# Performance work log

Hardware: AMD Instinct MI355X
Metric: run time of the kernel (lower is better)

## Reference

```python
import jax, jax.numpy as jnp
import numpy as np

ALPHA = 0.2  # LeakyReLU negative slope


def setup_inputs() -> dict:
    key = jax.random.key(0)
    k1, k2, k3, k4 = jax.random.split(key, 4)
    B, N, Fin, Fout = 8, 2048, 256, 256
    h = jax.random.normal(k1, (B, N, Fin), dtype=jnp.float32)
    # random 0/1 adjacency with guaranteed self-loops so every row has a neighbor
    adj = jax.random.randint(k2, (N, N), 0, 2).astype(jnp.float32)
    adj = jnp.maximum(adj, jnp.eye(N, dtype=jnp.float32))
    # xavier_uniform with gain=1.414
    def xavier(k, shape, gain=1.414):
        fan_in, fan_out = shape[0], shape[1]
        a = gain * np.sqrt(6.0 / (fan_in + fan_out))
        return jax.random.uniform(k, shape, dtype=jnp.float32, minval=-a, maxval=a)
    W = xavier(k3, (Fin, Fout))
    a = xavier(k4, (2 * Fout, 1))
    return {"h": h, "adj_matrix": adj, "W": W, "a": a}


def reference(h, adj_matrix, W, a):
    # h: [B, N, Fin], adj_matrix: [N, N], W: [Fin, Fout], a: [2*Fout, 1]
    Fout = W.shape[1]
    Wh = jnp.einsum("bnf,fo->bno", h, W)            # [B, N, Fout]
    a1, a2 = a[:Fout, 0], a[Fout:, 0]                 # split additive attention vector
    # e[b,i,j] = leakyrelu(Wh[b,i]@a1 + Wh[b,j]@a2) — equals concat([Wh_i,Wh_j])@a
    s1 = Wh @ a1                                      # [B, N]
    s2 = Wh @ a2                                      # [B, N]
    e = s1[:, :, None] + s2[:, None, :]               # [B, N, N]
    e = jnp.where(e >= 0, e, ALPHA * e)               # LeakyReLU
    e = jnp.where(adj_matrix[None] == 0, -jnp.inf, e)  # mask non-edges
    attention = jax.nn.softmax(e, axis=-1)            # [B, N, N]
    # dropout is identity in eval mode (training=False)
    h_prime = jnp.einsum("bij,bjo->bio", attention, Wh)
    return h_prime
```

## Files before the change

### kernel.cpp

```cpp
#include <hip/hip_runtime.h>
#include <cstdint>

#define NN 2048
#define LOG2E 1.4426950408889634f

typedef __attribute__((ext_vector_type(8))) short bf16x8;
typedef __attribute__((ext_vector_type(4))) float f32x4;

__device__ __forceinline__ unsigned short f2bf(float x){
  union { float f; unsigned u; } v; v.f = x;
  unsigned r = v.u + 0x7FFFu + ((v.u >> 16) & 1u);
  return (unsigned short)(r >> 16);
}
__device__ __forceinline__ unsigned pack2(float a, float b){
  return (unsigned)f2bf(a) | ((unsigned)f2bf(b) << 16);
}
__device__ __forceinline__ unsigned permpack(unsigned hi, unsigned lo){
  return __builtin_amdgcn_perm(hi, lo, 0x07060302u);
}

__global__ __launch_bounds__(256) void k_prep(const float* __restrict__ adj,
                                              const float* __restrict__ W,
                                              unsigned long long* __restrict__ ab,
                                              unsigned short* __restrict__ Wt){
  const int tid = threadIdx.x;
  const int bid = blockIdx.x;
  if (bid < 512){
    const int lane = tid & 63;
    unsigned* ab32 = (unsigned*)ab;
    #pragma unroll
    for (int r = 0; r < 4; r++){
      const int row = bid * 4 + r;
      #pragma unroll
      for (int part = 0; part < 2; part++){
        float4 v = ((const float4*)(adj + (size_t)row * NN))[part * 256 + tid];
        unsigned n = (v.x != 0.f ? 1u : 0u) | (v.y != 0.f ? 2u : 0u)
                   | (v.z != 0.f ? 4u : 0u) | (v.w != 0.f ? 8u : 0u);
        unsigned m;
        m = __shfl_xor(n, 1); n = (lane & 1) ? (m | (n << 4))  : (n | (m << 4));
        m = __shfl_xor(n, 2); n = (lane & 2) ? (m | (n << 8))  : (n | (m << 8));
        m = __shfl_xor(n, 4); n = (lane & 4) ? (m | (n << 16)) : (n | (m << 16));
        if ((lane & 7) == 0)
          ab32[row * 64 + part * 32 + (tid >> 3)] = n;
      }
    }
  } else {
    int g = (bid - 512) * 256 + tid;
    int o = g >> 8, k = g & 255;
    Wt[g] = f2bf(W[k * 256 + o]);
  }
}

__global__ __launch_bounds__(512, 2) void k_fused_gemm(const float* __restrict__ h,
                                                       const unsigned short* __restrict__ Wt,
                                                       const float* __restrict__ a,
                                                       unsigned short* __restrict__ WhT,
                                                       float* __restrict__ s1c,
                                                       float* __restrict__ s2c){
  __shared__ __align__(16) unsigned char As[2 * 8192];
  __shared__ __align__(16) unsigned short Ts[256 * 72];
  __shared__ float s1p[8][64], s2p[8][64];
  const int tid = threadIdx.x;
  const int r0 = blockIdx.x * 64;
  const int b  = r0 >> 11;
  const int i0 = r0 & (NN - 1);
  const int w = tid >> 6, lane = tid & 63, lhi = lane >> 4, llo = lane & 15;
  const int wc = w * 32;
  const int sit = w >> 1, skk = w & 1;
  const int srow = sit * 16 + llo;
  const int skol = skk * 32 + lhi * 8;

  f32x4 acc[4][2];
  #pragma unroll
  for (int i = 0; i < 4; i++)
    #pragma unroll
    for (int j = 0; j < 2; j++){ acc[i][j][0]=0.f; acc[i][j][1]=0.f; acc[i][j][2]=0.f; acc[i][j][3]=0.f; }

  float4 hv[4][2];
  #pragma unroll
  for (int t = 0; t < 4; t++){
    const float* hp = h + (size_t)(r0 + srow) * 256 + t * 64 + skol;
    hv[t][0] = *(const float4*)hp;
    hv[t][1] = *(const float4*)(hp + 4);
  }

  auto loadB = [&](int k0, bf16x8* dst){
    #pragma unroll
    for (int ot = 0; ot < 2; ot++)
      #pragma unroll
      for (int kk = 0; kk < 2; kk++)
        dst[ot * 2 + kk] = *(const bf16x8*)(Wt + (size_t)(wc + ot * 16 + llo) * 256 + k0 + kk * 32 + lhi * 8);
  };
  bf16x8 bfr[2][4];
  loadB(0, bfr[0]);

  #pragma unroll
  for (int t = 0; t < 4; t++){
    uint4 q = make_uint4(pack2(hv[t][0].x, hv[t][0].y), pack2(hv[t][0].z, hv[t][0].w),
                         pack2(hv[t][1].x, hv[t][1].y), pack2(hv[t][1].z, hv[t][1].w));
    *(uint4*)&As[(t & 1) * 8192 + w * 1024 + lane * 16] = q;
    __syncthreads();
    if (t < 3) loadB((t + 1) * 64, bfr[(t + 1) & 1]);
    bf16x8 af[2][4];
    #pragma unroll
    for (int kk = 0; kk < 2; kk++)
      #pragma unroll
      for (int it = 0; it < 4; it++)
        af[kk][it] = *(const bf16x8*)&As[(t & 1) * 8192 + (it * 2 + kk) * 1024 + lane * 16];
    #pragma unroll
    for (int kk = 0; kk < 2; kk++)
      #pragma unroll
      for (int it = 0; it < 4; it++)
        #pragma unroll
        for (int ot = 0; ot < 2; ot++)
          acc[it][ot] = __builtin_amdgcn_mfma_f32_16x16x32_bf16(af[kk][it], bfr[t & 1][ot * 2 + kk], acc[it][ot], 0, 0, 0);
  }

  float a1v[2], a2v[2];
  #pragma unroll
  for (int ot = 0; ot < 2; ot++){
    a1v[ot] = a[wc + ot * 16 + llo] * LOG2E;
    a2v[ot] = a[256 + wc + ot * 16 + llo] * LOG2E;
  }
  #pragma unroll
  for (int it = 0; it < 4; it++){
    #pragma unroll
    for (int q = 0; q < 4; q++){
      float p1 = acc[it][0][q] * a1v[0] + acc[it][1][q] * a1v[1];
      float p2 = acc[it][0][q] * a2v[0] + acc[it][1][q] * a2v[1];
      #pragma unroll
      for (int o = 1; o < 16; o <<= 1){ p1 += __shfl_xor(p1, o); p2 += __shfl_xor(p2, o); }
      if (llo == 0){
        s1p[w][it * 16 + lhi * 4 + q] = p1;
        s2p[w][it * 16 + lhi * 4 + q] = p2;
      }
    }
  }

  #pragma unroll
  for (int it = 0; it < 4; it++){
    #pragma unroll
    for (int ot = 0; ot < 2; ot++){
      int o = wc + ot * 16 + llo;
      uint2 u = make_uint2(pack2(acc[it][ot][0], acc[it][ot][1]),
                           pack2(acc[it][ot][2], acc[it][ot][3]));
      *(uint2*)&Ts[o * 72 + it * 16 + lhi * 4] = u;
    }
  }
  __syncthreads();

  if (tid < 64){
    float t1 = 0.f, t2 = 0.f;
    #pragma unroll
    for (int g = 0; g < 8; g++){ t1 += s1p[g][tid]; t2 += s2p[g][tid]; }
    s1c[r0 + tid] = t1;
    s2c[r0 + tid] = t2;
  }
  #pragma unroll
  for (int p = 0; p < 4; p++){
    int o = p * 64 + (tid >> 3), col = (tid & 7) * 8;
    *(uint4*)(WhT + (size_t)(b * 256 + o) * 2048 + i0 + col) = *(const uint4*)&Ts[o * 72 + col];
  }
}

__global__ __launch_bounds__(512, 2) void k_attn(const float* __restrict__ s1c,
                                                 const float* __restrict__ s2c,
                                                 const unsigned short* __restrict__ WhT,
                                                 const unsigned long long* __restrict__ ab,
                                                 float* __restrict__ out){
  __shared__ __align__(16) float E1s[2048];
  __shared__ __align__(16) float E2s[2048];
  __shared__ __align__(16) unsigned char PsB[2 * 16384];
  __shared__ __align__(16) unsigned char bitsB[64 * 264];
  __shared__ float s1s[64], lin[64], red[8], rsp[8][64];
  const int tid = threadIdx.x;
  const int bid = blockIdx.x;
  const int b = bid & 7, i0 = (bid >> 3) * 64;
  const int w = tid >> 6, lane = tid & 63, lhi = lane >> 4, llo = lane & 15;
  const int wc = w * 32;
  const int sit = w >> 1, skk = w & 1;
  const int sfrag = sit * 2 + skk;
  const int prow = sit * 16 + llo;

  float4 v = ((const float4*)(s2c + (size_t)b * NN))[tid];
  ((float4*)E1s)[tid] = make_float4(__builtin_amdgcn_exp2f(v.x), __builtin_amdgcn_exp2f(v.y),
                                    __builtin_amdgcn_exp2f(v.z), __builtin_amdgcn_exp2f(v.w));
  ((float4*)E2s)[tid] = make_float4(__builtin_amdgcn_exp2f(0.2f * v.x), __builtin_amdgcn_exp2f(0.2f * v.y),
                                    __builtin_amdgcn_exp2f(0.2f * v.z), __builtin_amdgcn_exp2f(0.2f * v.w));
  float vmax = fmaxf(fmaxf(v.x, v.y), fmaxf(v.z, v.w));
  #pragma unroll
  for (int o = 32; o; o >>= 1) vmax = fmaxf(vmax, __shfl_xor(vmax, o));
  if (lane == 0) red[w] = vmax;
  if (tid < 64) s1s[tid] = s1c[(size_t)b * NN + i0 + tid];
  #pragma unroll
  for (int k = 0; k < 4; k++){
    int g = k * 512 + tid;
    unsigned long long mw = ab[(size_t)i0 * 32 + g];
    *(unsigned long long*)&bitsB[(g >> 5) * 264 + (g & 31) * 8] = mw;
  }
  __syncthreads();
  float m2 = red[0];
  #pragma unroll
  for (int g = 1; g < 8; g++) m2 = fmaxf(m2, red[g]);

  const float s1v = s1s[prow];
  const float xm = s1v + m2;
  const float mv = fmaxf(xm, 0.2f * xm);
  const float k1 = __builtin_amdgcn_exp2f(s1v - mv);
  const float k2 = __builtin_amdgcn_exp2f(0.2f * s1v - mv);
  float rs = 0.f;

  f32x4 acc[4][2];
  #pragma unroll
  for (int i = 0; i < 4; i++)
    #pragma unroll
    for (int j = 0; j < 2; j++){ acc[i][j][0]=0.f; acc[i][j][1]=0.f; acc[i][j][2]=0.f; acc[i][j][3]=0.f; }

  auto loadB = [&](int j0, bf16x8* dst){
    #pragma unroll
    for (int jh = 0; jh < 2; jh++)
      #pragma unroll
      for (int ot = 0; ot < 2; ot++)
        #pragma unroll
        for (int kk = 0; kk < 2; kk++)
          dst[jh * 4 + ot * 2 + kk] = *(const bf16x8*)(WhT + (size_t)(b * 256 + wc + ot * 16 + llo) * 2048 + j0 + jh * 64 + kk * 32 + lhi * 8);
  };

  unsigned puq[8];
  auto computeP = [&](int tn, unsigned* pq){
    unsigned bits = bitsB[prow * 264 + tn * 8 + skk * 4 + lhi];
    const int off = tn * 64 + skk * 32 + lhi * 8;
    float4 xa = *(const float4*)&E1s[off];
    float4 xb = *(const float4*)&E1s[off + 4];
    float4 ya = *(const float4*)&E2s[off];
    float4 yb = *(const float4*)&E2s[off + 4];
    float e1[8] = {xa.x, xa.y, xa.z, xa.w, xb.x, xb.y, xb.z, xb.w};
    float e2[8] = {ya.x, ya.y, ya.z, ya.w, yb.x, yb.y, yb.z, yb.w};
    unsigned pu[8];
    #pragma unroll
    for (int e = 0; e < 8; e++){
      float p = fmaxf(e1[e] * k1, e2[e] * k2);
      unsigned m = ((bits >> e) & 1u) ? 0xFFFF0000u : 0u;
      unsigned u = __float_as_uint(p) & m;
      rs += __uint_as_float(u);
      pu[e] = u;
    }
    pq[0] = permpack(pu[1], pu[0]); pq[1] = permpack(pu[3], pu[2]);
    pq[2] = permpack(pu[5], pu[4]); pq[3] = permpack(pu[7], pu[6]);
  };

  auto stageBody = [&](int t, int BUF, bf16x8* curB, bf16x8* nxtB, bool last){
    *(uint4*)&PsB[BUF * 16384 +        sfrag * 1024 + lane * 16] = *(uint4*)&puq[0];
    *(uint4*)&PsB[BUF * 16384 + 8192 + sfrag * 1024 + lane * 16] = *(uint4*)&puq[4];
    __syncthreads();
    if (!last) loadB((t + 1) * 128, nxtB);
    bf16x8 af[2][4];
    #pragma unroll
    for (int kk = 0; kk < 2; kk++)
      #pragma unroll
      for (int it = 0; it < 4; it++)
        af[kk][it] = *(const bf16x8*)&PsB[BUF * 16384 + (it * 2 + kk) * 1024 + lane * 16];
    if (!last) computeP(2 * (t + 1), &puq[0]);
    #pragma unroll
    for (int kk = 0; kk < 2; kk++)
      #pragma unroll
      for (int it = 0; it < 4; it++)
        #pragma unroll
        for (int ot = 0; ot < 2; ot++)
          acc[it][ot] = __builtin_amdgcn_mfma_f32_16x16x32_bf16(af[kk][it], curB[ot * 2 + kk], acc[it][ot], 0, 0, 0);
    #pragma unroll
    for (int kk = 0; kk < 2; kk++)
      #pragma unroll
      for (int it = 0; it < 4; it++)
        af[kk][it] = *(const bf16x8*)&PsB[BUF * 16384 + 8192 + (it * 2 + kk) * 1024 + lane * 16];
    if (!last) computeP(2 * (t + 1) + 1, &puq[4]);
    #pragma unroll
    for (int kk = 0; kk < 2; kk++)
      #pragma unroll
      for (int it = 0; it < 4; it++)
        #pragma unroll
        for (int ot = 0; ot < 2; ot++)
          acc[it][ot] = __builtin_amdgcn_mfma_f32_16x16x32_bf16(af[kk][it], curB[4 + ot * 2 + kk], acc[it][ot], 0, 0, 0);
  };

  bf16x8 bA[8], bB[8];
  loadB(0, bA);
  computeP(0, &puq[0]);
  computeP(1, &puq[4]);
  for (int t2 = 0; t2 < 16; t2 += 2){
    stageBody(t2,     0, bA, bB, false);
    stageBody(t2 + 1, 1, bB, bA, t2 + 1 == 15);
  }

  rs += __shfl_xor(rs, 16);
  rs += __shfl_xor(rs, 32);
  if (lhi == 0) rsp[w][prow] = rs;
  __syncthreads();
  if (tid < 64){
    int it = tid >> 4;
    lin[tid] = 1.0f / (rsp[it * 2][tid] + rsp[it * 2 + 1][tid]);
  }
  __syncthreads();

  #pragma unroll
  for (int it = 0; it < 4; it++){
    #pragma unroll
    for (int ot = 0; ot < 2; ot++){
      int col = wc + ot * 16 + llo;
      #pragma unroll
      for (int q = 0; q < 4; q++){
        int row = it * 16 + lhi * 4 + q;
        out[(size_t)(b * NN + i0 + row) * 256 + col] = acc[it][ot][q] * lin[row];
      }
    }
  }
}

extern "C" void kernel_launch(void* const* d_in, const int* in_sizes, int n_in,
                              void* d_out, int out_size, void* d_ws, size_t ws_size,
                              hipStream_t stream) {
  const float* h   = (const float*)d_in[0];
  const float* adj = (const float*)d_in[1];
  const float* W   = (const float*)d_in[2];
  const float* a   = (const float*)d_in[3];
  float* out = (float*)d_out;

  char* ws = (char*)d_ws;
  unsigned short* WhT      = (unsigned short*)(ws);
  unsigned short* Wt       = (unsigned short*)(ws + 8388608);
  unsigned long long* ab   = (unsigned long long*)(ws + 8519680);
  float* s1c               = (float*)(ws + 9043968);
  float* s2c               = (float*)(ws + 9109504);

  hipLaunchKernelGGL(k_prep,       dim3(768), dim3(256), 0, stream, adj, W, ab, Wt);
  hipLaunchKernelGGL(k_fused_gemm, dim3(256), dim3(512), 0, stream, h, Wt, a, WhT, s1c, s2c);
  hipLaunchKernelGGL(k_attn,       dim3(256), dim3(512), 0, stream, s1c, s2c, WhT, ab, out);
}
```

Baseline: 132.7 us.

## Stage 512 attention columns per barrier and prioritize MFMA issue

The P-tile staging buffer in shared memory grows to hold 512 key columns at once, so the block synchronizes 4 times instead of 16. Eight P fragments are computed per stage and kept in registers, while WhT fragments are double-buffered at 64-column granularity. The first B load is hoisted above the prologue, and s_setprio raises wave priority around the MFMA bursts. In exchange it uses much more LDS (64KB for Ps) and more registers for puq, which could limit occupancy or cause spills.

After: 130.9 us. No clear change (-1.4%).

```diff
diff --git a/kernel.cpp b/kernel.cpp
--- a/kernel.cpp
+++ b/kernel.cpp
@@ -170,7 +170,7 @@
                                                  float* __restrict__ out){
   __shared__ __align__(16) float E1s[2048];
   __shared__ __align__(16) float E2s[2048];
-  __shared__ __align__(16) unsigned char PsB[2 * 16384];
+  __shared__ __align__(16) unsigned char Ps[65536];
   __shared__ __align__(16) unsigned char bitsB[64 * 264];
   __shared__ float s1s[64], lin[64], red[8], rsp[8][64];
   const int tid = threadIdx.x;
@@ -182,6 +182,16 @@
   const int sfrag = sit * 2 + skk;
   const int prow = sit * 16 + llo;
 
+  auto loadB = [&](int j0, bf16x8* dst){
+    #pragma unroll
+    for (int ot = 0; ot < 2; ot++)
+      #pragma unroll
+      for (int kk = 0; kk < 2; kk++)
+        dst[ot * 2 + kk] = *(const bf16x8*)(WhT + (size_t)(b * 256 + wc + ot * 16 + llo) * 2048 + j0 + kk * 32 + lhi * 8);
+  };
+  bf16x8 bA[4], bB[4];
+  loadB(0, bA);
+
   float4 v = ((const float4*)(s2c + (size_t)b * NN))[tid];
   ((float4*)E1s)[tid] = make_float4(__builtin_amdgcn_exp2f(v.x), __builtin_amdgcn_exp2f(v.y),
                                     __builtin_amdgcn_exp2f(v.z), __builtin_amdgcn_exp2f(v.w));
@@ -216,24 +226,14 @@
     #pragma unroll
     for (int j = 0; j < 2; j++){ acc[i][j][0]=0.f; acc[i][j][1]=0.f; acc[i][j][2]=0.f; acc[i][j][3]=0.f; }
 
-  auto loadB = [&](int j0, bf16x8* dst){
-    #pragma unroll
-    for (int jh = 0; jh < 2; jh++)
-      #pragma unroll
-      for (int ot = 0; ot < 2; ot++)
-        #pragma unroll
-        for (int kk = 0; kk < 2; kk++)
-          dst[jh * 4 + ot * 2 + kk] = *(const bf16x8*)(WhT + (size_t)(b * 256 + wc + ot * 16 + llo) * 2048 + j0 + jh * 64 + kk * 32 + lhi * 8);
-  };
-
-  unsigned puq[8];
-  auto computeP = [&](int tn, unsigned* pq){
-    unsigned bits = bitsB[prow * 264 + tn * 8 + skk * 4 + lhi];
-    const int off = tn * 64 + skk * 32 + lhi * 8;
-    float4 xa = *(const float4*)&E1s[off];
-    float4 xb = *(const float4*)&E1s[off + 4];
-    float4 ya = *(const float4*)&E2s[off];
-    float4 yb = *(const float4*)&E2s[off + 4];
+  unsigned puq[32];
+  auto computeP = [&](int sN, int jc, unsigned* pq){
+    const int j0 = sN * 512 + jc * 64 + skk * 32 + lhi * 8;
+    unsigned bits = bitsB[prow * 264 + (j0 >> 3)];
+    float4 xa = *(const float4*)&E1s[j0];
+    float4 xb = *(const float4*)&E1s[j0 + 4];
+    float4 ya = *(const float4*)&E2s[j0];
+    float4 yb = *(const float4*)&E2s[j0 + 4];
     float e1[8] = {xa.x, xa.y, xa.z, xa.w, xb.x, xb.y, xb.z, xb.w};
     float e2[8] = {ya.x, ya.y, ya.z, ya.w, yb.x, yb.y, yb.z, yb.w};
     unsigned pu[8];
@@ -249,47 +249,38 @@
     pq[2] = permpack(pu[5], pu[4]); pq[3] = permpack(pu[7], pu[6]);
   };
 
-  auto stageBody = [&](int t, int BUF, bf16x8* curB, bf16x8* nxtB, bool last){
-    *(uint4*)&PsB[BUF * 16384 +        sfrag * 1024 + lane * 16] = *(uint4*)&puq[0];
-    *(uint4*)&PsB[BUF * 16384 + 8192 + sfrag * 1024 + lane * 16] = *(uint4*)&puq[4];
+  #pragma unroll
+  for (int jc = 0; jc < 8; jc++) computeP(0, jc, &puq[jc * 4]);
+
+  for (int s = 0; s < 4; s++){
+    if (s) __syncthreads();
+    #pragma unroll
+    for (int jc = 0; jc < 8; jc++)
+      *(uint4*)&Ps[jc * 8192 + sfrag * 1024 + lane * 16] = *(const uint4*)&puq[jc * 4];
     __syncthreads();
-    if (!last) loadB((t + 1) * 128, nxtB);
-    bf16x8 af[2][4];
-    #pragma unroll
-    for (int kk = 0; kk < 2; kk++)
-      #pragma unroll
-      for (int it = 0; it < 4; it++)
-        af[kk][it] = *(const bf16x8*)&PsB[BUF * 16384 + (it * 2 + kk) * 1024 + lane * 16];
-    if (!last) computeP(2 * (t + 1), &puq[0]);
-    #pragma unroll
-    for (int kk = 0; kk < 2; kk++)
-      #pragma unroll
-      for (int it = 0; it < 4; it++)
+    #pragma unroll
+    for (int jc = 0; jc < 8; jc++){
+      bf16x8 af[2][4];
+      #pragma unroll
+      for (int kk = 0; kk < 2; kk++)
         #pragma unroll
-        for (int ot = 0; ot < 2; ot++)
-          acc[it][ot] = __builtin_amdgcn_mfma_f32_16x16x32_bf16(af[kk][it], curB[ot * 2 + kk], acc[it][ot], 0, 0, 0);
-    #pragma unroll
-    for (int kk = 0; kk < 2; kk++)
-      #pragma unroll
-      for (int it = 0; it < 4; it++)
-        af[kk][it] = *(const bf16x8*)&PsB[BUF * 16384 + 8192 + (it * 2 + kk) * 1024 + lane * 16];
-    if (!last) computeP(2 * (t + 1) + 1, &puq[4]);
-    #pragma unroll
-    for (int kk = 0; kk < 2; kk++)
-      #pragma unroll
-      for (int it = 0; it < 4; it++)
+        for (int it = 0; it < 4; it++)
+          af[kk][it] = *(const bf16x8*)&Ps[jc * 8192 + (it * 2 + kk) * 1024 + lane * 16];
+      bf16x8* cur = (jc & 1) ? bB : bA;
+      bf16x8* nxt = (jc & 1) ? bA : bB;
+      if (jc < 7)       loadB((s * 8 + jc + 1) * 64, nxt);
+      else if (s < 3)   loadB((s + 1) * 512, nxt);
+      if (s < 3) computeP(s + 1, jc, &puq[jc * 4]);
+      __builtin_amdgcn_s_setprio(1);
+      #pragma unroll
+      for (int kk = 0; kk < 2; kk++)
         #pragma unroll
-        for (int ot = 0; ot < 2; ot++)
-          acc[it][ot] = __builtin_amdgcn_mfma_f32_16x16x32_bf16(af[kk][it], curB[4 + ot * 2 + kk], acc[it][ot], 0, 0, 0);
-  };
-
-  bf16x8 bA[8], bB[8];
-  loadB(0, bA);
-  computeP(0, &puq[0]);
-  computeP(1, &puq[4]);
-  for (int t2 = 0; t2 < 16; t2 += 2){
-    stageBody(t2,     0, bA, bB, false);
-    stageBody(t2 + 1, 1, bB, bA, t2 + 1 == 15);
+        for (int it = 0; it < 4; it++)
+          #pragma unroll
+          for (int ot = 0; ot < 2; ot++)
+            acc[it][ot] = __builtin_amdgcn_mfma_f32_16x16x32_bf16(af[kk][it], cur[ot * 2 + kk], acc[it][ot], 0, 0, 0);
+      __builtin_amdgcn_s_setprio(0);
+    }
   }
 
   rs += __shfl_xor(rs, 16);
```
